# Optimization experiments

Measured on AMD Instinct MI355X. Metric: run time of the kernel, lower is better.

The kernel has to match this reference:

```python
import jax, jax.numpy as jnp
import numpy as np

L = 248      # max_clip_seq_len
WIN = 3      # window_size
H = 8        # attention heads
D = 768      # input/output dim
HID = 256    # rope hidden dim
SIGMA = 2.0
EPS_LN = 1e-5


def _layernorm(x, g, b):
    m = jnp.mean(x, axis=-1, keepdims=True)
    v = jnp.var(x, axis=-1, keepdims=True)
    return (x - m) / jnp.sqrt(v + EPS_LN) * g + b


def _normalize(x):
    n = jnp.linalg.norm(x, axis=-1, keepdims=True)
    return x / jnp.maximum(n, 1e-12)


def _peb_forward(word_feat, text_feat_full, word_pos, ctx_W, ctx_b, in_W, in_b,
                 out_W, out_b, cn_g, cn_b, r1_W, r1_b, ln_g, ln_b, r2_W, r2_b,
                 pos_emb, pos_temp):
    B, N, _ = word_feat.shape
    valid = word_pos != -1                              # [B,N] bool
    vf = valid.astype(word_feat.dtype)[..., None]       # [B,N,1]
    wp = jnp.clip(word_pos, 0, L - 1)                   # [B,N]
    half = WIN // 2
    offs = jnp.arange(-half, half + 1)
    positions = jnp.clip(wp[..., None] + offs[None, None, :], 0, L - 1)
    ctx = text_feat_full[jnp.arange(B)[:, None, None], positions]
    ctx_anchor = (ctx.reshape(B, N, WIN * D) @ ctx_W + ctx_b) * vf       # [B,N,D]
    q = word_feat * vf                                  # word_proj is Identity (768->768)
    # MultiheadAttention (batch_first), query=q, key=value=ctx_anchor
    hd = D // H
    qp = (q @ in_W[:, :D] + in_b[:D]).reshape(B, N, H, hd)
    kp = (ctx_anchor @ in_W[:, D:2 * D] + in_b[D:2 * D]).reshape(B, N, H, hd)
    vp = (ctx_anchor @ in_W[:, 2 * D:] + in_b[2 * D:]).reshape(B, N, H, hd)
    scores = jnp.einsum('bqhd,bkhd->bhqk', qp, kp) / jnp.sqrt(jnp.asarray(hd, q.dtype))
    attn = jax.nn.softmax(scores, axis=-1)
    ao = jnp.einsum('bhqk,bkhd->bqhd', attn, vp).reshape(B, N, D)
    attn_out = ao @ out_W + out_b
    x = _layernorm(q + attn_out, cn_g, cn_b) * vf       # word_feat_with_ctx
    # rope_mapping: Linear -> GELU -> LayerNorm -> Linear
    rope = _layernorm(jax.nn.gelu(x @ r1_W + r1_b, approximate=False), ln_g, ln_b) @ r2_W + r2_b
    rope_n = _normalize(rope)
    clip_ref_n = _normalize(pos_emb)                    # [L,D]
    temp = jnp.maximum(pos_temp, 0.001)
    logits = jnp.einsum('bnd,ld->bnl', rope_n, clip_ref_n) / temp
    log_q = jax.nn.log_softmax(logits, axis=-1)
    # gaussian soft target over L positions
    pos_idx = jnp.arange(L, dtype=jnp.float32)
    d2 = (pos_idx[None, None, :] - wp[..., None].astype(jnp.float32)) ** 2
    targ = jnp.exp(-d2 / (2.0 * SIGMA ** 2))
    targ = targ / (targ.sum(axis=-1, keepdims=True) + 1e-12)
    lqv = log_q * vf
    tv = targ * vf
    n_valid = valid.sum().astype(jnp.float32)
    safe_t = jnp.where(tv > 0, tv, 1.0)
    kl = jnp.sum(jnp.where(tv > 0, tv * (jnp.log(safe_t) - lqv), 0.0)) / (n_valid + 1e-12)
    # relative position loss on cosine similarity
    pos_sim01 = (jnp.einsum('bnd,bmd->bnm', rope_n, rope_n) + 1.0) / 2.0
    wpf = wp.astype(jnp.float32)
    target_sim = 1.0 - jnp.abs(wpf[:, :, None] - wpf[:, None, :]) / float(L)
    vm2 = vf[:, :, 0][:, None, :] * vf[:, :, 0][:, :, None]
    rel = jnp.sum((pos_sim01 * vm2 - target_sim * vm2) ** 2) / (vm2.sum() + 1e-12)
    peb_loss = (1.0 * kl + 0.5 * rel) * 1.0             # kl_weight=1, rel_weight=0.5, peb_weight=1
    # scatter blended positional features to 248-length sequence (vectorized over batch)
    vals = 0.8 * pos_emb[wp] + 0.2 * rope               # [B,N,D]
    pos_s = jnp.where(valid, wp, L)                     # invalid -> OOB index, dropped
    emb = jnp.zeros((B, L, D), word_feat.dtype).at[jnp.arange(B)[:, None], pos_s].set(vals, mode='drop')
    return emb, peb_loss, kl, rel


def setup_inputs() -> dict:
    key = jax.random.key(0)
    ks = jax.random.split(key, 20)
    B, N = 128, 128
    word_feat = jax.random.normal(ks[0], (B, N, D), jnp.float32)
    text_feat_full = jax.random.normal(ks[1], (B, L, D), jnp.float32)
    # unique sorted positions per batch (scatter is then deterministic, matching torch)
    perms = jax.vmap(lambda k: jax.random.permutation(k, L))(jax.random.split(ks[2], B))
    word_pos = jnp.sort(perms[:, :N], axis=-1).astype(jnp.int32)
    s = 0.02
    return {
        'word_feat': word_feat,
        'text_feat_full': text_feat_full,
        'word_pos': word_pos,
        'ctx_W': s * jax.random.normal(ks[3], (WIN * D, D), jnp.float32),
        'ctx_b': s * jax.random.normal(ks[4], (D,), jnp.float32),
        'in_W': s * jax.random.normal(ks[5], (D, 3 * D), jnp.float32),
        'in_b': s * jax.random.normal(ks[6], (3 * D,), jnp.float32),
        'out_W': s * jax.random.normal(ks[7], (D, D), jnp.float32),
        'out_b': s * jax.random.normal(ks[8], (D,), jnp.float32),
        'cn_g': jnp.ones((D,), jnp.float32) + s * jax.random.normal(ks[9], (D,), jnp.float32),
        'cn_b': s * jax.random.normal(ks[10], (D,), jnp.float32),
        'r1_W': s * jax.random.normal(ks[11], (D, HID), jnp.float32),
        'r1_b': s * jax.random.normal(ks[12], (HID,), jnp.float32),
        'ln_g': jnp.ones((HID,), jnp.float32) + s * jax.random.normal(ks[13], (HID,), jnp.float32),
        'ln_b': s * jax.random.normal(ks[14], (HID,), jnp.float32),
        'r2_W': s * jax.random.normal(ks[15], (HID, D), jnp.float32),
        'r2_b': s * jax.random.normal(ks[16], (D,), jnp.float32),
        'pos_emb': jax.random.normal(ks[17], (L, D), jnp.float32),
        'pos_temp': jnp.asarray(1.0, jnp.float32),
    }


def reference(word_feat, text_feat_full, word_pos, ctx_W, ctx_b, in_W, in_b,
              out_W, out_b, cn_g, cn_b, r1_W, r1_b, ln_g, ln_b, r2_W, r2_b,
              pos_emb, pos_temp):
    return _peb_forward(word_feat, text_feat_full, word_pos, ctx_W, ctx_b, in_W, in_b,
                        out_W, out_b, cn_g, cn_b, r1_W, r1_b, ln_g, ln_b, r2_W, r2_b,
                        pos_emb, pos_temp)
```

## Files before the change

kernel.cpp:

```cpp
#include <hip/hip_runtime.h>
#include <math.h>

#define BB   128
#define NN   128
#define LL   248
#define DD   768
#define HH   8
#define HDh  96
#define HIDN 256
#define MROWS (BB*NN)
#define MB_   (1u<<20)
#define KVLD 1536

typedef unsigned short u16;
typedef unsigned int   u32;
typedef __attribute__((ext_vector_type(8))) short s16x8;
typedef __attribute__((ext_vector_type(4))) float f32x4;

__device__ __forceinline__ u16 f2bf(float x) {
    u32 u = __float_as_uint(x);
    u32 r = u + 0x7fffu + ((u >> 16) & 1u);
    return (u16)(r >> 16);
}
__device__ __forceinline__ float bf2f(u16 h) {
    return __uint_as_float(((u32)h) << 16);
}
__device__ __forceinline__ void gload16(const void* g, void* l) {
    __builtin_amdgcn_global_load_lds(
        (const __attribute__((address_space(1))) void*)g,
        (__attribute__((address_space(3))) void*)l, 16, 0, 0);
}

template<int NT>
__device__ __forceinline__ float breduce_sum(float v, float* red) {
    const int tid = threadIdx.x;
    red[tid] = v; __syncthreads();
#pragma unroll
    for (int o = NT / 2; o > 0; o >>= 1) {
        if (tid < o) red[tid] += red[tid + o];
        __syncthreads();
    }
    float r = red[0]; __syncthreads();
    return r;
}
__device__ __forceinline__ double breduce_sum_d256(double v, double* red) {
    const int tid = threadIdx.x;
    red[tid] = v; __syncthreads();
#pragma unroll
    for (int o = 128; o > 0; o >>= 1) {
        if (tid < o) red[tid] += red[tid + o];
        __syncthreads();
    }
    double r = red[0]; __syncthreads();
    return r;
}

#define TEXT_F4 (BB*LL*DD/4)
#define Q_F4    (MROWS*(DD/4))
__global__ __launch_bounds__(256)
void prep_all_kernel(const float* __restrict__ ctx_W, u16* __restrict__ ctx_Wt,
                     const float* __restrict__ in_W,  u16* __restrict__ in_Wt,
                     const float* __restrict__ out_W, u16* __restrict__ out_Wt,
                     const float* __restrict__ r1_W,  u16* __restrict__ r1_Wt,
                     const float* __restrict__ r2_W,  u16* __restrict__ r2_Wt,
                     const float* __restrict__ text,  u16* __restrict__ textb,
                     const float* __restrict__ wf,    u16* __restrict__ qb,
                     const int* __restrict__ wpos,    int* __restrict__ cpos,
                     const float* __restrict__ pe,    u16* __restrict__ clipb,
                     float* __restrict__ zbias) {
    __shared__ float smem[32 * 33];
    int bid = blockIdx.x;
    const int tid = threadIdx.x;

    if (bid < 4416) {
        const float* src; u16* dst; int C;
        if (bid < 1728)      { src = ctx_W; dst = ctx_Wt; C = 768;  }
        else if (bid < 3456) { src = in_W;  dst = in_Wt;  C = 2304; bid -= 1728; }
        else if (bid < 4032) { src = out_W; dst = out_Wt; C = 768;  bid -= 3456; }
        else if (bid < 4224) { src = r1_W;  dst = r1_Wt;  C = 256;  bid -= 4032; }
        else                 { src = r2_W;  dst = r2_Wt;  C = 768;  bid -= 4224; }
        const int R = (C == 768) ? ((dst == ctx_Wt) ? 2304 : ((dst == out_Wt) ? 768 : 256))
                                 : 768;
        const int ct = C >> 5;
        const int r0 = (bid / ct) * 32, c0 = (bid % ct) * 32;
        const int tx = tid & 31, ty = tid >> 5;
#pragma unroll
        for (int i = 0; i < 32; i += 8)
            smem[(ty + i) * 33 + tx] = src[(size_t)(r0 + ty + i) * C + c0 + tx];
        __syncthreads();
#pragma unroll
        for (int i = 0; i < 32; i += 8)
            dst[(size_t)(c0 + ty + i) * R + r0 + tx] = f2bf(smem[tx * 33 + ty + i]);
    } else if (bid < 4672) {
        const int l = bid - 4416;
        if (l >= LL) {
            for (int j = 0; j < 3; ++j) clipb[(size_t)l * DD + tid + j * 256] = 0;
            return;
        }
        float t[3]; float q = 0.f;
#pragma unroll
        for (int j = 0; j < 3; ++j) {
            t[j] = pe[(size_t)l * DD + tid + j * 256];
            q = fmaf(t[j], t[j], q);
        }
        q = breduce_sum<256>(q, smem);
        float inv = 1.f / fmaxf(sqrtf(q), 1e-12f);
#pragma unroll
        for (int j = 0; j < 3; ++j)
            clipb[(size_t)l * DD + tid + j * 256] = f2bf(t[j] * inv);
    } else {
        const int ebid = bid - 4672;
        if (ebid == 0) {
            for (int r = tid; r < MROWS; r += 256) {
                int w = wpos[r];
                cpos[r] = w < 0 ? 0 : (w > LL - 1 ? LL - 1 : w);
            }
            if (tid < 256) zbias[tid] = 0.f;
        }
        const int lane = tid & 63;
        const int wid = ebid * 4 + (tid >> 6);
        const int NCHUNK = (TEXT_F4 + Q_F4) / 512;
        for (int c = wid; c < NCHUNK; c += 8192) {
            const int base = c * 512;
            if (base < TEXT_F4) {
                const float4* sp = (const float4*)text;
                uint2* op = (uint2*)textb;
                float4 v[8];
#pragma unroll
                for (int j = 0; j < 8; ++j)
                    v[j] = sp[(size_t)base + j * 64 + lane];
#pragma unroll
                for (int j = 0; j < 8; ++j) {
                    uint2 o;
                    o.x = (u32)f2bf(v[j].x) | ((u32)f2bf(v[j].y) << 16);
                    o.y = (u32)f2bf(v[j].z) | ((u32)f2bf(v[j].w) << 16);
                    op[(size_t)base + j * 64 + lane] = o;
                }
            } else {
                const int qb4 = base - TEXT_F4;
                const float4* sp = (const float4*)wf;
                uint2* op = (uint2*)qb;
                float4 v[8]; float vfm[8];
#pragma unroll
                for (int j = 0; j < 8; ++j)
                    v[j] = sp[(size_t)qb4 + j * 64 + lane];
#pragma unroll
                for (int j = 0; j < 8; ++j)
                    vfm[j] = (wpos[(qb4 + j * 64 + lane) / 192] != -1) ? 1.f : 0.f;
#pragma unroll
                for (int j = 0; j < 8; ++j) {
                    uint2 o;
                    o.x = (u32)f2bf(v[j].x * vfm[j]) | ((u32)f2bf(v[j].y * vfm[j]) << 16);
                    o.y = (u32)f2bf(v[j].z * vfm[j]) | ((u32)f2bf(v[j].w * vfm[j]) << 16);
                    op[(size_t)qb4 + j * 64 + lane] = o;
                }
            }
        }
    }
}

template<int GATHER, int CBF16, int MASK>
__global__ __launch_bounds__(256)
void gemm_bt(const u16* __restrict__ A,
             const u16* __restrict__ TXT,
             const int* __restrict__ cpos,
             const u16* __restrict__ Bt,
             const float* __restrict__ bias,
             void* __restrict__ Cout, int ldc, int K,
             const int* __restrict__ wpos) {
    __shared__ __align__(16) u16 Alds[128 * 64];
    __shared__ __align__(16) u16 Blds[128 * 64];
    const int tid = threadIdx.x;
    const int l = tid & 63, wv = tid >> 6;

    const int gx  = gridDim.x;
    const int hw  = blockIdx.y * gx + blockIdx.x;
    const int nwg = gx * gridDim.y;
    const int cpx = nwg >> 3;
    const int lin = (hw & 7) * cpx + (hw >> 3);
    const int m0 = (lin / gx) * 128, n0 = (lin % gx) * 128;

    const int rw = wv * 8 + (l >> 3);
    const int ce = ((l & 7) ^ (l >> 3)) << 3;
    u16* Ad0 = Alds + wv * 512;
    u16* Bd0 = Blds + wv * 512;

    const int wm = (wv >> 1) * 64, wn = (wv & 1) * 64;
    const int la = l & 15, lg = l >> 4;

    int aoff[4], boff[4];
#pragma unroll
    for (int m = 0; m < 4; ++m) {
        int ra = wm + m * 16 + la;
        aoff[m] = ra * 64 + (((lg ^ (la & 7)) << 3));
        int rb = wn + m * 16 + la;
        boff[m] = rb * 64 + (((lg ^ (la & 7)) << 3));
    }

    const u16* pb[4];
#pragma unroll
    for (int i = 0; i < 4; ++i)
        pb[i] = Bt + (size_t)(n0 + rw + i * 32) * K + ce;

    f32x4 acc[4][4] = {};

    auto do_step = [&](const u16* a0, const u16* a1, const u16* a2, const u16* a3,
                       const u16* b0, const u16* b1, const u16* b2, const u16* b3) {
        gload16(a0, Ad0);
        gload16(a1, Ad0 + 2048);
        gload16(a2, Ad0 + 4096);
        gload16(a3, Ad0 + 6144);
        gload16(b0, Bd0);
        gload16(b1, Bd0 + 2048);
        gload16(b2, Bd0 + 4096);
        gload16(b3, Bd0 + 6144);
        __syncthreads();
#pragma unroll
        for (int kk = 0; kk < 2; ++kk) {
            const int kx = kk << 5;
            s16x8 af[4], bf[4];
#pragma unroll
            for (int m = 0; m < 4; ++m) af[m] = *(const s16x8*)(Alds + (aoff[m] ^ kx));
#pragma unroll
            for (int n = 0; n < 4; ++n) bf[n] = *(const s16x8*)(Blds + (boff[n] ^ kx));
#pragma unroll
            for (int m = 0; m < 4; ++m)
#pragma unroll
                for (int n = 0; n < 4; ++n)
                    acc[m][n] = __builtin_amdgcn_mfma_f32_16x16x32_bf16(
                        af[m], bf[n], acc[m][n], 0, 0, 0);
        }
        __syncthreads();
    };

    if constexpr (GATHER) {
        int gb[4], gc[4];
#pragma unroll
        for (int i = 0; i < 4; ++i) {
            int g = m0 + rw + i * 32;
            gb[i] = g >> 7;
            gc[i] = cpos[g];
        }
#pragma unroll 1
        for (int w = 0; w < 3; ++w) {
            const u16* pa[4];
#pragma unroll
            for (int i = 0; i < 4; ++i) {
                int p = gc[i] + w - 1;
                p = p < 0 ? 0 : (p > LL - 1 ? LL - 1 : p);
                pa[i] = TXT + ((size_t)(gb[i] * LL + p)) * DD + ce;
            }
            const u16* b0 = pb[0] + w * DD; const u16* b1 = pb[1] + w * DD;
            const u16* b2 = pb[2] + w * DD; const u16* b3 = pb[3] + w * DD;
#pragma unroll 1
            for (int kt = 0; kt < 12; ++kt)
                do_step(pa[0] + kt * 64, pa[1] + kt * 64, pa[2] + kt * 64, pa[3] + kt * 64,
                        b0 + kt * 64, b1 + kt * 64, b2 + kt * 64, b3 + kt * 64);
        }
    } else {
        const u16* pa[4];
#pragma unroll
        for (int i = 0; i < 4; ++i)
            pa[i] = A + (size_t)(m0 + rw + i * 32) * K + ce;
        const int nk = K >> 6;
#pragma unroll 1
        for (int kt = 0; kt < nk; ++kt)
            do_step(pa[0] + (kt << 6), pa[1] + (kt << 6), pa[2] + (kt << 6), pa[3] + (kt << 6),
                    pb[0] + (kt << 6), pb[1] + (kt << 6), pb[2] + (kt << 6), pb[3] + (kt << 6));
    }

#pragma unroll
    for (int m = 0; m < 4; ++m) {
        const int rb = m0 + wm + m * 16 + lg * 4;
        float vf[4];
        if constexpr (MASK) {
#pragma unroll
            for (int r = 0; r < 4; ++r) vf[r] = (wpos[rb + r] != -1) ? 1.f : 0.f;
        }
#pragma unroll
        for (int n = 0; n < 4; ++n) {
            const int col = n0 + wn + n * 16 + la;
            const float bv = bias[col];
#pragma unroll
            for (int r = 0; r < 4; ++r) {
                float o = acc[m][n][r] + bv;
                if constexpr (MASK) o *= vf[r];
                if constexpr (CBF16)
                    ((u16*)Cout)[(size_t)(rb + r) * ldc + col] = f2bf(o);
                else
                    ((float*)Cout)[(size_t)(rb + r) * ldc + col] = o;
            }
        }
    }
}

__global__ __launch_bounds__(512)
void attn_mfma_kernel(const u16* __restrict__ qp, const u16* __restrict__ kvb,
                      u16* __restrict__ ao) {
    __shared__ __align__(16) u16 K_lds[128 * 96];
    __shared__ __align__(16) u16 Vt_lds[96 * 128];
    __shared__ __align__(16) u16 P_lds[128 * 128];
    const int bh = blockIdx.x;
    const int b = bh >> 3, h = bh & 7;
    const int tid = threadIdx.x;
    const int l = tid & 63, wv = tid >> 6;
    const int la = l & 15, lg = l >> 4;
    const float scale = 0.10206207261596575f;

    const size_t qbase  = ((size_t)b * NN) * DD + h * HDh;
    const size_t kvbase = ((size_t)b * NN) * KVLD + h * HDh;

#pragma unroll
    for (int i = 0; i < 3; ++i) {
        int f = i * 8192 + wv * 1024 + l * 16;
        int row = f / 192;
        int inner = f - row * 192;
        gload16((const char*)(kvb + kvbase + (size_t)row * KVLD) + inner,
                (char*)K_lds + f);
    }

    uint4 vchunk[3]; int vkey[3], vd0[3];
#pragma unroll
    for (int i = 0; i < 3; ++i) {
        int c = tid + i * 512;
        int key = c / 12, dc = c - key * 12;
        vkey[i] = key; vd0[i] = dc * 8;
        vchunk[i] = *(const uint4*)(kvb + kvbase + (size_t)key * KVLD + DD + dc * 8);
    }

    const int q0 = wv * 16;
    s16x8 qf[3];
#pragma unroll
    for (int kt = 0; kt < 3; ++kt)
        qf[kt] = *(const s16x8*)(qp + qbase + (size_t)(q0 + la) * DD + kt * 32 + lg * 8);

#pragma unroll
    for (int i = 0; i < 3; ++i) {
        const u16* e = (const u16*)&vchunk[i];
#pragma unroll
        for (int j = 0; j < 8; ++j) {
            int d = vd0[i] + j;
            int byte = ((d * 128 + vkey[i]) * 2) ^ ((d & 7) << 4);
            *(u16*)((char*)Vt_lds + byte) = e[j];
        }
    }
    __syncthreads();

    f32x4 sacc[8] = {};
#pragma unroll
    for (int kt = 0; kt < 3; ++kt) {
#pragma unroll
        for (int nf = 0; nf < 8; ++nf) {
            s16x8 bfr = *(const s16x8*)(K_lds + (nf * 16 + la) * 96 + kt * 32 + lg * 8);
            sacc[nf] = __builtin_amdgcn_mfma_f32_16x16x32_bf16(qf[kt], bfr, sacc[nf], 0, 0, 0);
        }
    }

#pragma unroll
    for (int r = 0; r < 4; ++r) {
        float m = -1e30f;
#pragma unroll
        for (int nf = 0; nf < 8; ++nf) m = fmaxf(m, sacc[nf][r]);
#pragma unroll
        for (int o = 8; o > 0; o >>= 1) m = fmaxf(m, __shfl_xor(m, o, 64));
        m *= scale;
        float p[8]; float s = 0.f;
#pragma unroll
        for (int nf = 0; nf < 8; ++nf) { p[nf] = expf(sacc[nf][r] * scale - m); s += p[nf]; }
#pragma unroll
        for (int o = 8; o > 0; o >>= 1) s += __shfl_xor(s, o, 64);
        const float inv = 1.f / s;
        const int q = q0 + lg * 4 + r;
#pragma unroll
        for (int nf = 0; nf < 8; ++nf) {
            int byte = ((q * 128 + nf * 16 + la) * 2) ^ ((q & 7) << 4);
            *(u16*)((char*)P_lds + byte) = f2bf(p[nf] * inv);
        }
    }
    __syncthreads();

    f32x4 oacc[6] = {};
#pragma unroll
    for (int kk = 0; kk < 4; ++kk) {
        const int qrow = q0 + la;
        int abyte = ((qrow * 128 + kk * 32 + lg * 8) * 2) ^ ((qrow & 7) << 4);
        s16x8 af = *(const s16x8*)((char*)P_lds + abyte);
#pragma unroll
        for (int nf = 0; nf < 6; ++nf) {
            const int d = nf * 16 + la;
            int bbyte = ((d * 128 + kk * 32 + lg * 8) * 2) ^ ((d & 7) << 4);
            s16x8 bfr = *(const s16x8*)((char*)Vt_lds + bbyte);
            oacc[nf] = __builtin_amdgcn_mfma_f32_16x16x32_bf16(af, bfr, oacc[nf], 0, 0, 0);
        }
    }

#pragma unroll
    for (int nf = 0; nf < 6; ++nf) {
#pragma unroll
        for (int r = 0; r < 4; ++r) {
            const int q = q0 + lg * 4 + r;
            ao[qbase + (size_t)q * DD + nf * 16 + la] = f2bf(oacc[nf][r]);
        }
    }
}

__global__ __launch_bounds__(256)
void ln768_kernel(const u16* __restrict__ qb, const u16* __restrict__ at,
                  const int* __restrict__ wpos, const float* __restrict__ g,
                  const float* __restrict__ bta, u16* __restrict__ xout) {
    __shared__ float red[256];
    const int r = blockIdx.x, tid = threadIdx.x;
    const float vf = (wpos[r] != -1) ? 1.f : 0.f;
    float t[3]; float s = 0.f, q = 0.f;
#pragma unroll
    for (int j = 0; j < 3; ++j) {
        int d = tid + j * 256;
        t[j] = bf2f(qb[(size_t)r * DD + d]) + bf2f(at[(size_t)r * DD + d]);
        s += t[j];
        q = fmaf(t[j], t[j], q);
    }
    s = breduce_sum<256>(s, red);
    q = breduce_sum<256>(q, red);
    float mean = s * (1.f / DD);
    float var  = q * (1.f / DD) - mean * mean;
    float inv  = 1.f / sqrtf(var + 1e-5f);
#pragma unroll
    for (int j = 0; j < 3; ++j) {
        int d = tid + j * 256;
        xout[(size_t)r * DD + d] = f2bf(((t[j] - mean) * inv * g[d] + bta[d]) * vf);
    }
}

__global__ __launch_bounds__(256)
void ln256_gelu_kernel(const u16* __restrict__ g1, const float* __restrict__ lg,
                       const float* __restrict__ lb, u16* __restrict__ hout) {
    __shared__ float red[256];
    const int r = blockIdx.x, tid = threadIdx.x;
    float v  = bf2f(g1[(size_t)r * HIDN + tid]);
    float ge = 0.5f * v * (1.f + erff(v * 0.7071067811865475f));
    float s = breduce_sum<256>(ge, red);
    float q = breduce_sum<256>(ge * ge, red);
    float mean = s * (1.f / HIDN);
    float var  = q * (1.f / HIDN) - mean * mean;
    float inv  = 1.f / sqrtf(var + 1e-5f);
    hout[(size_t)r * HIDN + tid] = f2bf((ge - mean) * inv * lg[tid] + lb[tid]);
}

__global__ __launch_bounds__(256)
void norm_rnb_kernel(const u16* __restrict__ ropeb, u16* __restrict__ rnb) {
    __shared__ float red[256];
    const int r = blockIdx.x, tid = threadIdx.x;
    float t[3]; float q = 0.f;
#pragma unroll
    for (int j = 0; j < 3; ++j) {
        t[j] = bf2f(ropeb[(size_t)r * DD + tid + j * 256]);
        q = fmaf(t[j], t[j], q);
    }
    q = breduce_sum<256>(q, red);
    float inv = 1.f / fmaxf(sqrtf(q), 1e-12f);
#pragma unroll
    for (int j = 0; j < 3; ++j)
        rnb[(size_t)r * DD + tid + j * 256] = f2bf(t[j] * inv);
}

__global__ __launch_bounds__(256)
void emb_full_kernel(const u16* __restrict__ ropeb, const float* __restrict__ pe,
                     const int* __restrict__ wpos, float* __restrict__ emb) {
    const int bl = blockIdx.x;
    const int b = bl / LL, l = bl - b * LL;
    const int tid = threadIdx.x;
    const int* wp = wpos + b * NN;
    int lo = 0, hi = NN - 1, found = -1;
    while (lo <= hi) {
        int mid = (lo + hi) >> 1;
        int v = wp[mid];
        if (v == l) { found = mid; break; }
        if (v < l) lo = mid + 1; else hi = mid - 1;
    }
    float* dst = emb + (size_t)bl * DD;
    if (found >= 0) {
        const u16* rr = ropeb + (size_t)(b * NN + found) * DD;
#pragma unroll
        for (int j = 0; j < 3; ++j) {
            int d = tid + j * 256;
            dst[d] = 0.8f * pe[(size_t)l * DD + d] + 0.2f * bf2f(rr[d]);
        }
    } else {
#pragma unroll
        for (int j = 0; j < 3; ++j)
            dst[tid + j * 256] = 0.f;
    }
}

__global__ __launch_bounds__(256)
void kl_lite_kernel(const float* __restrict__ logits, const int* __restrict__ wpos,
                    const float* __restrict__ pos_temp, float* __restrict__ klp) {
    const int row = blockIdx.x * 4 + (threadIdx.x >> 6);
    const int l = threadIdx.x & 63;
    const float invt = 1.f / fmaxf(pos_temp[0], 0.001f);
    const float* lrow = logits + (size_t)row * 256;

    float lg[4];
#pragma unroll
    for (int q = 0; q < 4; ++q) {
        int c = l + q * 64;
        lg[q] = (c < LL) ? lrow[c] * invt : -1e30f;
    }
    float m = fmaxf(fmaxf(lg[0], lg[1]), fmaxf(lg[2], lg[3]));
#pragma unroll
    for (int o = 32; o > 0; o >>= 1) m = fmaxf(m, __shfl_xor(m, o, 64));

    float S = 0.f;
#pragma unroll
    for (int q = 0; q < 4; ++q) S += expf(lg[q] - m);
#pragma unroll
    for (int o = 32; o > 0; o >>= 1) S += __shfl_xor(S, o, 64);
    const float logZ = m + logf(S);

    const int wr = wpos[row];
    const bool valid = (wr != -1);
    const int wp = wr < 0 ? 0 : (wr > LL - 1 ? LL - 1 : wr);

    float targ[4]; float tsum = 0.f;
#pragma unroll
    for (int q = 0; q < 4; ++q) {
        int c = l + q * 64;
        float dl = (float)c - (float)wp;
        targ[q] = (c < LL) ? expf(-dl * dl * 0.125f) : 0.f;
        tsum += targ[q];
    }
#pragma unroll
    for (int o = 32; o > 0; o >>= 1) tsum += __shfl_xor(tsum, o, 64);
    const float tden = 1.f / (tsum + 1e-12f);

    float c_ = 0.f;
#pragma unroll
    for (int q = 0; q < 4; ++q) {
        float tn = targ[q] * tden;
        if (valid && tn > 0.f) c_ += tn * (logf(tn) - (lg[q] - logZ));
    }
#pragma unroll
    for (int o = 32; o > 0; o >>= 1) c_ += __shfl_xor(c_, o, 64);
    if (l == 0) klp[row] = c_;
}

__global__ __launch_bounds__(512)
void rel_mfma_kernel(const u16* __restrict__ rnb, const int* __restrict__ wpos,
                     float* __restrict__ rel_part, float* __restrict__ vm2_part) {
    __shared__ __align__(16) u16 T[128 * 32];
    __shared__ float red[512];
    const int blk = blockIdx.x;
    const int b = blk >> 1, jh = blk & 1;
    const int tid = threadIdx.x;
    const int l = tid & 63, wv = tid >> 6;
    const int la = l & 15, lg = l >> 4;

    const int f = wv * 1024 + l * 16;
    const int rA = f >> 6;
    const int cb = (f & 63) ^ (((rA >> 1) & 3) << 4);
    const int ce = cb >> 1;
    const u16* src = rnb + ((size_t)(b * NN + rA)) * DD + ce;
    u16* dst = T + wv * 512;

    const int ra = wv * 16 + la;
    const int aoff = ra * 32 + ((lg * 8) ^ (((ra >> 1) & 3) << 3));
    int boff[4];
#pragma unroll
    for (int nf = 0; nf < 4; ++nf) {
        int rb = jh * 64 + nf * 16 + la;
        boff[nf] = rb * 32 + ((lg * 8) ^ (((rb >> 1) & 3) << 3));
    }

    f32x4 acc[4] = {};
    for (int kt = 0; kt < 24; ++kt) {
        gload16(src + kt * 32, dst);
        __syncthreads();
        s16x8 a = *(const s16x8*)(T + aoff);
        s16x8 bf_[4];
#pragma unroll
        for (int nf = 0; nf < 4; ++nf) bf_[nf] = *(const s16x8*)(T + boff[nf]);
#pragma unroll
        for (int nf = 0; nf < 4; ++nf)
            acc[nf] = __builtin_amdgcn_mfma_f32_16x16x32_bf16(a, bf_[nf], acc[nf], 0, 0, 0);
        __syncthreads();
    }

    float wif[4], vi[4];
#pragma unroll
    for (int r = 0; r < 4; ++r) {
        int wi = wpos[b * NN + wv * 16 + lg * 4 + r];
        vi[r] = (wi != -1) ? 1.f : 0.f;
        wif[r] = (float)(wi < 0 ? 0 : (wi > LL - 1 ? LL - 1 : wi));
    }
    float csum = 0.f, msum = 0.f;
#pragma unroll
    for (int nf = 0; nf < 4; ++nf) {
        int wj = wpos[b * NN + jh * 64 + nf * 16 + la];
        float vj = (wj != -1) ? 1.f : 0.f;
        float wjf = (float)(wj < 0 ? 0 : (wj > LL - 1 ? LL - 1 : wj));
#pragma unroll
        for (int r = 0; r < 4; ++r) {
            float sim = (acc[nf][r] + 1.f) * 0.5f;
            float ts  = 1.f - fabsf(wif[r] - wjf) * (1.f / (float)LL);
            float m2  = vi[r] * vj;
            float df  = m2 * (sim - ts);
            csum += df * df;
            msum += m2;
        }
    }
    csum = breduce_sum<512>(csum, red);
    msum = breduce_sum<512>(msum, red);
    if (tid == 0) { rel_part[blk] = csum; vm2_part[blk] = msum; }
}

__global__ __launch_bounds__(256)
void final_kernel(const float* __restrict__ klp, const float* __restrict__ relp,
                  const float* __restrict__ vmp, const int* __restrict__ wpos,
                  float* __restrict__ outs) {
    __shared__ double rd[256];
    const int tid = threadIdx.x;
    double kl = 0.0, rel = 0.0, vm = 0.0, nv = 0.0;
    for (int r = tid; r < MROWS; r += 256) {
        kl += (double)klp[r];
        nv += (wpos[r] != -1) ? 1.0 : 0.0;
    }
    if (tid < 256) {
        rel += (double)relp[tid];
        vm  += (double)vmp[tid];
    }
    kl  = breduce_sum_d256(kl, rd);
    rel = breduce_sum_d256(rel, rd);
    vm  = breduce_sum_d256(vm, rd);
    nv  = breduce_sum_d256(nv, rd);
    if (tid == 0) {
        float klf  = (float)(kl / (nv + 1e-12));
        float relf = (float)(rel / (vm + 1e-12));
        outs[0] = klf + 0.5f * relf;
        outs[1] = klf;
        outs[2] = relf;
    }
}

extern "C" void kernel_launch(void* const* d_in, const int* in_sizes, int n_in,
                              void* d_out, int out_size, void* d_ws, size_t ws_size,
                              hipStream_t stream) {
    (void)in_sizes; (void)n_in; (void)ws_size; (void)out_size;

    const float* word_feat = (const float*)d_in[0];
    const float* text      = (const float*)d_in[1];
    const int*   wpos      = (const int*)d_in[2];
    const float* ctx_W     = (const float*)d_in[3];
    const float* ctx_b     = (const float*)d_in[4];
    const float* in_W      = (const float*)d_in[5];
    const float* in_b      = (const float*)d_in[6];
    const float* out_W     = (const float*)d_in[7];
    const float* out_b     = (const float*)d_in[8];
    const float* cn_g      = (const float*)d_in[9];
    const float* cn_b      = (const float*)d_in[10];
    const float* r1_W      = (const float*)d_in[11];
    const float* r1_b      = (const float*)d_in[12];
    const float* ln_g      = (const float*)d_in[13];
    const float* ln_b      = (const float*)d_in[14];
    const float* r2_W      = (const float*)d_in[15];
    const float* r2_b      = (const float*)d_in[16];
    const float* pos_emb   = (const float*)d_in[17];
    const float* pos_temp  = (const float*)d_in[18];

    char* W = (char*)d_ws;
    u16*   ctx_Wt = (u16*)(W);
    u16*   in_Wt  = ctx_Wt + (size_t)768 * 2304;
    u16*   out_Wt = in_Wt  + (size_t)2304 * 768;
    u16*   r1_Wt  = out_Wt + (size_t)768 * 768;
    u16*   r2_Wt  = r1_Wt  + (size_t)256 * 768;
    u16*   clipb  = r2_Wt + (size_t)768 * 256;
    int*   cposb  = (int*)(clipb + (size_t)256 * DD);
    float* klp    = (float*)(cposb + MROWS);
    float* relp   = klp + MROWS;
    float* vmp    = relp + 256;
    float* zbias  = vmp + 256;
    u16*   textb  = (u16*)(W + (size_t)12 * MB_);
    u16*   atoutb = textb;
    float* logits = (float*)(W + (size_t)12 * MB_);
    u16*   xb     = (u16*)(W + (size_t)36 * MB_);
    u16*   qb     = (u16*)(W + (size_t)60 * MB_);
    u16*   ctxa   = (u16*)(W + (size_t)86 * MB_);
    u16*   aob    = ctxa;
    u16*   rnb    = ctxa;
    u16*   qpb    = (u16*)(W + (size_t)112 * MB_);
    u16*   g1b    = (u16*)(W + (size_t)112 * MB_);
    u16*   hb     = (u16*)(W + (size_t)128 * MB_);
    u16*   kvb    = (u16*)(W + (size_t)138 * MB_);
    u16*   ropeb  = kvb;

    dim3 blk(256);

    prep_all_kernel<<<dim3(4416 + 256 + 2048), blk, 0, stream>>>(
        ctx_W, ctx_Wt, in_W, in_Wt, out_W, out_Wt, r1_W, r1_Wt, r2_W, r2_Wt,
        text, textb, word_feat, qb, wpos, cposb, pos_emb, clipb, zbias);

    dim3 g768(6, 128);
    dim3 g1536(12, 128);
    dim3 g256(2, 128);

    gemm_bt<1, 1, 1><<<g768, blk, 0, stream>>>(
        nullptr, textb, cposb, ctx_Wt, ctx_b, ctxa, DD, 3 * DD, wpos);
    gemm_bt<0, 1, 0><<<g768, blk, 0, stream>>>(
        qb, nullptr, nullptr, in_Wt, in_b, qpb, DD, DD, nullptr);
    gemm_bt<0, 1, 0><<<g1536, blk, 0, stream>>>(
        ctxa, nullptr, nullptr, in_Wt + (size_t)768 * 768, in_b + DD, kvb, KVLD, DD, nullptr);
    attn_mfma_kernel<<<dim3(BB * HH), dim3(512), 0, stream>>>(qpb, kvb, aob);
    gemm_bt<0, 1, 0><<<g768, blk, 0, stream>>>(
        aob, nullptr, nullptr, out_Wt, out_b, atoutb, DD, DD, nullptr);
    ln768_kernel<<<dim3(MROWS), blk, 0, stream>>>(qb, atoutb, wpos, cn_g, cn_b, xb);
    gemm_bt<0, 1, 0><<<g256, blk, 0, stream>>>(
        xb, nullptr, nullptr, r1_Wt, r1_b, g1b, HIDN, DD, nullptr);
    ln256_gelu_kernel<<<dim3(MROWS), blk, 0, stream>>>(g1b, ln_g, ln_b, hb);
    gemm_bt<0, 1, 0><<<g768, blk, 0, stream>>>(
        hb, nullptr, nullptr, r2_Wt, r2_b, ropeb, DD, HIDN, nullptr);
    norm_rnb_kernel<<<dim3(MROWS), blk, 0, stream>>>(ropeb, rnb);
    gemm_bt<0, 0, 0><<<g256, blk, 0, stream>>>(
        rnb, nullptr, nullptr, clipb, zbias, logits, 256, DD, nullptr);
    kl_lite_kernel<<<dim3(MROWS / 4), blk, 0, stream>>>(logits, wpos, pos_temp, klp);
    rel_mfma_kernel<<<dim3(BB * 2), dim3(512), 0, stream>>>(rnb, wpos, relp, vmp);
    emb_full_kernel<<<dim3(BB * LL), blk, 0, stream>>>(
        ropeb, pos_emb, wpos, (float*)d_out);
    final_kernel<<<dim3(1), blk, 0, stream>>>(
        klp, relp, vmp, wpos, (float*)d_out + (size_t)BB * LL * DD);
}
```

Before: 447.9 us.

## Merge independent kernels into shared launches to fill the GPU

Three pairs of independent kernels now share a launch, with the block index choosing the work: the ctx and q-projection GEMMs, row normalization with the embedding output, and the logits GEMM with the relation-similarity reduction. The relation kernel moves from 512 to 256 threads and each wave handles two 16-row groups. The aim is to cut launch count and fill idle CUs when single small GEMMs leave the machine underused. The cost is the heterogeneous blocks imbalancing each other, and the emb write now runs before the logits rather than overlapping later work.

```diff
diff --git a/kernel.cpp b/kernel.cpp
--- a/kernel.cpp
+++ b/kernel.cpp
@@ -160,25 +160,18 @@
 }
 
 template<int GATHER, int CBF16, int MASK>
-__global__ __launch_bounds__(256)
-void gemm_bt(const u16* __restrict__ A,
-             const u16* __restrict__ TXT,
-             const int* __restrict__ cpos,
-             const u16* __restrict__ Bt,
-             const float* __restrict__ bias,
-             void* __restrict__ Cout, int ldc, int K,
-             const int* __restrict__ wpos) {
-    __shared__ __align__(16) u16 Alds[128 * 64];
-    __shared__ __align__(16) u16 Blds[128 * 64];
+__device__ __forceinline__ void gemm_tile(
+    const int m0, const int n0,
+    const u16* __restrict__ A,
+    const u16* __restrict__ TXT,
+    const int* __restrict__ cpos,
+    const u16* __restrict__ Bt,
+    const float* __restrict__ bias,
+    void* __restrict__ Cout, int ldc, int K,
+    const int* __restrict__ wpos,
+    u16* Alds, u16* Blds) {
     const int tid = threadIdx.x;
     const int l = tid & 63, wv = tid >> 6;
-
-    const int gx  = gridDim.x;
-    const int hw  = blockIdx.y * gx + blockIdx.x;
-    const int nwg = gx * gridDim.y;
-    const int cpx = nwg >> 3;
-    const int lin = (hw & 7) * cpx + (hw >> 3);
-    const int m0 = (lin / gx) * 128, n0 = (lin % gx) * 128;
 
     const int rw = wv * 8 + (l >> 3);
     const int ce = ((l & 7) ^ (l >> 3)) << 3;
@@ -291,6 +284,152 @@
                     ((float*)Cout)[(size_t)(rb + r) * ldc + col] = o;
             }
         }
+    }
+}
+
+template<int GATHER, int CBF16, int MASK>
+__global__ __launch_bounds__(256)
+void gemm_bt(const u16* __restrict__ A,
+             const u16* __restrict__ TXT,
+             const int* __restrict__ cpos,
+             const u16* __restrict__ Bt,
+             const float* __restrict__ bias,
+             void* __restrict__ Cout, int ldc, int K,
+             const int* __restrict__ wpos) {
+    __shared__ __align__(16) u16 Alds[128 * 64];
+    __shared__ __align__(16) u16 Blds[128 * 64];
+    const int gx  = gridDim.x;
+    const int hw  = blockIdx.y * gx + blockIdx.x;
+    const int nwg = gx * gridDim.y;
+    const int cpx = nwg >> 3;
+    const int lin = (hw & 7) * cpx + (hw >> 3);
+    const int m0 = (lin / gx) * 128, n0 = (lin % gx) * 128;
+    gemm_tile<GATHER, CBF16, MASK>(m0, n0, A, TXT, cpos, Bt, bias,
+                                   Cout, ldc, K, wpos, Alds, Blds);
+}
+
+__global__ __launch_bounds__(256)
+void gemm_ctx_qp_kernel(const u16* __restrict__ textb, const int* __restrict__ cpos,
+                        const u16* __restrict__ ctx_Wt, const float* __restrict__ ctx_b,
+                        u16* __restrict__ ctxa,
+                        const u16* __restrict__ qb, const u16* __restrict__ in_Wt,
+                        const float* __restrict__ in_b, u16* __restrict__ qpb,
+                        const int* __restrict__ wpos) {
+    __shared__ __align__(16) u16 Alds[128 * 64];
+    __shared__ __align__(16) u16 Blds[128 * 64];
+    const int bid = blockIdx.x;
+    if (bid < 768) {
+        const int lin = (bid & 7) * 96 + (bid >> 3);
+        const int m0 = (lin / 6) * 128, n0 = (lin % 6) * 128;
+        gemm_tile<1, 1, 1>(m0, n0, nullptr, textb, cpos, ctx_Wt, ctx_b,
+                           ctxa, DD, 3 * DD, wpos, Alds, Blds);
+    } else {
+        const int b2 = bid - 768;
+        const int lin = (b2 & 7) * 96 + (b2 >> 3);
+        const int m0 = (lin / 6) * 128, n0 = (lin % 6) * 128;
+        gemm_tile<0, 1, 0>(m0, n0, qb, nullptr, nullptr, in_Wt, in_b,
+                           qpb, DD, DD, nullptr, Alds, Blds);
+    }
+}
+
+__device__ __forceinline__ void rel_tile(int blk, const u16* __restrict__ rnb,
+                                         const int* __restrict__ wpos,
+                                         float* __restrict__ rel_part,
+                                         float* __restrict__ vm2_part,
+                                         u16* T ) {
+    float* red = (float*)(T + 4096);
+    const int b = blk >> 1, jh = blk & 1;
+    const int tid = threadIdx.x;
+    const int l = tid & 63, wv = tid >> 6;
+    const int la = l & 15, lg = l >> 4;
+
+    const int f0 = wv * 1024 + l * 16;
+    const int f1 = f0 + 4096;
+    const int rA0 = f0 >> 6, rA1 = f1 >> 6;
+    const int ce0 = ((f0 & 63) ^ (((rA0 >> 1) & 3) << 4)) >> 1;
+    const int ce1 = ((f1 & 63) ^ (((rA1 >> 1) & 3) << 4)) >> 1;
+    const u16* src0 = rnb + ((size_t)(b * NN + rA0)) * DD + ce0;
+    const u16* src1 = rnb + ((size_t)(b * NN + rA1)) * DD + ce1;
+    u16* dst0 = T + wv * 512;
+    u16* dst1 = T + 2048 + wv * 512;
+
+    int aoff[2];
+#pragma unroll
+    for (int g = 0; g < 2; ++g) {
+        int ra = wv * 32 + g * 16 + la;
+        aoff[g] = ra * 32 + ((lg * 8) ^ (((ra >> 1) & 3) << 3));
+    }
+    int boff[4];
+#pragma unroll
+    for (int nf = 0; nf < 4; ++nf) {
+        int rb = jh * 64 + nf * 16 + la;
+        boff[nf] = rb * 32 + ((lg * 8) ^ (((rb >> 1) & 3) << 3));
+    }
+
+    f32x4 acc[2][4] = {};
+    for (int kt = 0; kt < 24; ++kt) {
+        gload16(src0 + kt * 32, dst0);
+        gload16(src1 + kt * 32, dst1);
+        __syncthreads();
+        s16x8 a[2], bf_[4];
+#pragma unroll
+        for (int g = 0; g < 2; ++g) a[g] = *(const s16x8*)(T + aoff[g]);
+#pragma unroll
+        for (int nf = 0; nf < 4; ++nf) bf_[nf] = *(const s16x8*)(T + boff[nf]);
+#pragma unroll
+        for (int g = 0; g < 2; ++g)
+#pragma unroll
+            for (int nf = 0; nf < 4; ++nf)
+                acc[g][nf] = __builtin_amdgcn_mfma_f32_16x16x32_bf16(
+                    a[g], bf_[nf], acc[g][nf], 0, 0, 0);
+        __syncthreads();
+    }
+
+    float csum = 0.f, msum = 0.f;
+#pragma unroll
+    for (int g = 0; g < 2; ++g) {
+        float wif[4], vi[4];
+#pragma unroll
+        for (int r = 0; r < 4; ++r) {
+            int wi = wpos[b * NN + wv * 32 + g * 16 + lg * 4 + r];
+            vi[r] = (wi != -1) ? 1.f : 0.f;
+            wif[r] = (float)(wi < 0 ? 0 : (wi > LL - 1 ? LL - 1 : wi));
+        }
+#pragma unroll
+        for (int nf = 0; nf < 4; ++nf) {
+            int wj = wpos[b * NN + jh * 64 + nf * 16 + la];
+            float vj = (wj != -1) ? 1.f : 0.f;
+            float wjf = (float)(wj < 0 ? 0 : (wj > LL - 1 ? LL - 1 : wj));
+#pragma unroll
+            for (int r = 0; r < 4; ++r) {
+                float sim = (acc[g][nf][r] + 1.f) * 0.5f;
+                float ts  = 1.f - fabsf(wif[r] - wjf) * (1.f / (float)LL);
+                float m2  = vi[r] * vj;
+                float df  = m2 * (sim - ts);
+                csum += df * df;
+                msum += m2;
+            }
+        }
+    }
+    csum = breduce_sum<256>(csum, red);
+    msum = breduce_sum<256>(msum, red);
+    if (tid == 0) { rel_part[blk] = csum; vm2_part[blk] = msum; }
+}
+
+__global__ __launch_bounds__(256)
+void logits_rel_kernel(const u16* __restrict__ rnb, const u16* __restrict__ clipb,
+                       const float* __restrict__ zbias, float* __restrict__ logits,
+                       const int* __restrict__ wpos,
+                       float* __restrict__ relp, float* __restrict__ vmp) {
+    __shared__ __align__(16) u16 pool[2 * 128 * 64];
+    const int bid = blockIdx.x;
+    if (bid < 256) {
+        const int lin = (bid & 7) * 32 + (bid >> 3);
+        const int m0 = (lin >> 1) * 128, n0 = (lin & 1) * 128;
+        gemm_tile<0, 0, 0>(m0, n0, rnb, nullptr, nullptr, clipb, zbias,
+                           logits, 256, DD, nullptr, pool, pool + 128 * 64);
+    } else {
+        rel_tile(bid - 256, rnb, wpos, relp, vmp, pool);
     }
 }
 
@@ -447,48 +586,49 @@
 }
 
 __global__ __launch_bounds__(256)
-void norm_rnb_kernel(const u16* __restrict__ ropeb, u16* __restrict__ rnb) {
+void norm_emb_kernel(const u16* __restrict__ ropeb, const float* __restrict__ pe,
+                     const int* __restrict__ wpos, u16* __restrict__ rnb,
+                     float* __restrict__ emb) {
     __shared__ float red[256];
-    const int r = blockIdx.x, tid = threadIdx.x;
-    float t[3]; float q = 0.f;
-#pragma unroll
-    for (int j = 0; j < 3; ++j) {
-        t[j] = bf2f(ropeb[(size_t)r * DD + tid + j * 256]);
-        q = fmaf(t[j], t[j], q);
-    }
-    q = breduce_sum<256>(q, red);
-    float inv = 1.f / fmaxf(sqrtf(q), 1e-12f);
-#pragma unroll
-    for (int j = 0; j < 3; ++j)
-        rnb[(size_t)r * DD + tid + j * 256] = f2bf(t[j] * inv);
-}
-
-__global__ __launch_bounds__(256)
-void emb_full_kernel(const u16* __restrict__ ropeb, const float* __restrict__ pe,
-                     const int* __restrict__ wpos, float* __restrict__ emb) {
-    const int bl = blockIdx.x;
-    const int b = bl / LL, l = bl - b * LL;
+    const int bid = blockIdx.x;
     const int tid = threadIdx.x;
-    const int* wp = wpos + b * NN;
-    int lo = 0, hi = NN - 1, found = -1;
-    while (lo <= hi) {
-        int mid = (lo + hi) >> 1;
-        int v = wp[mid];
-        if (v == l) { found = mid; break; }
-        if (v < l) lo = mid + 1; else hi = mid - 1;
-    }
-    float* dst = emb + (size_t)bl * DD;
-    if (found >= 0) {
-        const u16* rr = ropeb + (size_t)(b * NN + found) * DD;
+    if (bid < MROWS) {
+        const int r = bid;
+        float t[3]; float q = 0.f;
 #pragma unroll
         for (int j = 0; j < 3; ++j) {
-            int d = tid + j * 256;
-            dst[d] = 0.8f * pe[(size_t)l * DD + d] + 0.2f * bf2f(rr[d]);
-        }
+            t[j] = bf2f(ropeb[(size_t)r * DD + tid + j * 256]);
+            q = fmaf(t[j], t[j], q);
+        }
+        q = breduce_sum<256>(q, red);
+        float inv = 1.f / fmaxf(sqrtf(q), 1e-12f);
+#pragma unroll
+        for (int j = 0; j < 3; ++j)
+            rnb[(size_t)r * DD + tid + j * 256] = f2bf(t[j] * inv);
     } else {
-#pragma unroll
-        for (int j = 0; j < 3; ++j)
-            dst[tid + j * 256] = 0.f;
+        const int bl = bid - MROWS;
+        const int b = bl / LL, l = bl - b * LL;
+        const int* wp = wpos + b * NN;
+        int lo = 0, hi = NN - 1, found = -1;
+        while (lo <= hi) {
+            int mid = (lo + hi) >> 1;
+            int v = wp[mid];
+            if (v == l) { found = mid; break; }
+            if (v < l) lo = mid + 1; else hi = mid - 1;
+        }
+        float* dst = emb + (size_t)bl * DD;
+        if (found >= 0) {
+            const u16* rr = ropeb + (size_t)(b * NN + found) * DD;
+#pragma unroll
+            for (int j = 0; j < 3; ++j) {
+                int d = tid + j * 256;
+                dst[d] = 0.8f * pe[(size_t)l * DD + d] + 0.2f * bf2f(rr[d]);
+            }
+        } else {
+#pragma unroll
+            for (int j = 0; j < 3; ++j)
+                dst[tid + j * 256] = 0.f;
+        }
     }
 }
 
@@ -542,75 +682,6 @@
 #pragma unroll
     for (int o = 32; o > 0; o >>= 1) c_ += __shfl_xor(c_, o, 64);
     if (l == 0) klp[row] = c_;
-}
-
-__global__ __launch_bounds__(512)
-void rel_mfma_kernel(const u16* __restrict__ rnb, const int* __restrict__ wpos,
-                     float* __restrict__ rel_part, float* __restrict__ vm2_part) {
-    __shared__ __align__(16) u16 T[128 * 32];
-    __shared__ float red[512];
-    const int blk = blockIdx.x;
-    const int b = blk >> 1, jh = blk & 1;
-    const int tid = threadIdx.x;
-    const int l = tid & 63, wv = tid >> 6;
-    const int la = l & 15, lg = l >> 4;
-
-    const int f = wv * 1024 + l * 16;
-    const int rA = f >> 6;
-    const int cb = (f & 63) ^ (((rA >> 1) & 3) << 4);
-    const int ce = cb >> 1;
-    const u16* src = rnb + ((size_t)(b * NN + rA)) * DD + ce;
-    u16* dst = T + wv * 512;
-
-    const int ra = wv * 16 + la;
-    const int aoff = ra * 32 + ((lg * 8) ^ (((ra >> 1) & 3) << 3));
-    int boff[4];
-#pragma unroll
-    for (int nf = 0; nf < 4; ++nf) {
-        int rb = jh * 64 + nf * 16 + la;
-        boff[nf] = rb * 32 + ((lg * 8) ^ (((rb >> 1) & 3) << 3));
-    }
-
-    f32x4 acc[4] = {};
-    for (int kt = 0; kt < 24; ++kt) {
-        gload16(src + kt * 32, dst);
-        __syncthreads();
-        s16x8 a = *(const s16x8*)(T + aoff);
-        s16x8 bf_[4];
-#pragma unroll
-        for (int nf = 0; nf < 4; ++nf) bf_[nf] = *(const s16x8*)(T + boff[nf]);
-#pragma unroll
-        for (int nf = 0; nf < 4; ++nf)
-            acc[nf] = __builtin_amdgcn_mfma_f32_16x16x32_bf16(a, bf_[nf], acc[nf], 0, 0, 0);
-        __syncthreads();
-    }
-
-    float wif[4], vi[4];
-#pragma unroll
-    for (int r = 0; r < 4; ++r) {
-        int wi = wpos[b * NN + wv * 16 + lg * 4 + r];
-        vi[r] = (wi != -1) ? 1.f : 0.f;
-        wif[r] = (float)(wi < 0 ? 0 : (wi > LL - 1 ? LL - 1 : wi));
-    }
-    float csum = 0.f, msum = 0.f;
-#pragma unroll
-    for (int nf = 0; nf < 4; ++nf) {
-        int wj = wpos[b * NN + jh * 64 + nf * 16 + la];
-        float vj = (wj != -1) ? 1.f : 0.f;
-        float wjf = (float)(wj < 0 ? 0 : (wj > LL - 1 ? LL - 1 : wj));
-#pragma unroll
-        for (int r = 0; r < 4; ++r) {
-            float sim = (acc[nf][r] + 1.f) * 0.5f;
-            float ts  = 1.f - fabsf(wif[r] - wjf) * (1.f / (float)LL);
-            float m2  = vi[r] * vj;
-            float df  = m2 * (sim - ts);
-            csum += df * df;
-            msum += m2;
-        }
-    }
-    csum = breduce_sum<512>(csum, red);
-    msum = breduce_sum<512>(msum, red);
-    if (tid == 0) { rel_part[blk] = csum; vm2_part[blk] = msum; }
 }
 
 __global__ __launch_bounds__(256)
@@ -700,30 +771,25 @@
 
     dim3 g768(6, 128);
     dim3 g1536(12, 128);
-    dim3 g256(2, 128);
-
-    gemm_bt<1, 1, 1><<<g768, blk, 0, stream>>>(
-        nullptr, textb, cposb, ctx_Wt, ctx_b, ctxa, DD, 3 * DD, wpos);
-    gemm_bt<0, 1, 0><<<g768, blk, 0, stream>>>(
-        qb, nullptr, nullptr, in_Wt, in_b, qpb, DD, DD, nullptr);
+
+    gemm_ctx_qp_kernel<<<dim3(1536), blk, 0, stream>>>(
+        textb, cposb, ctx_Wt, ctx_b, ctxa, qb, in_Wt, in_b, qpb, wpos);
     gemm_bt<0, 1, 0><<<g1536, blk, 0, stream>>>(
         ctxa, nullptr, nullptr, in_Wt + (size_t)768 * 768, in_b + DD, kvb, KVLD, DD, nullptr);
     attn_mfma_kernel<<<dim3(BB * HH), dim3(512), 0, stream>>>(qpb, kvb, aob);
     gemm_bt<0, 1, 0><<<g768, blk, 0, stream>>>(
         aob, nullptr, nullptr, out_Wt, out_b, atoutb, DD, DD, nullptr);
     ln768_kernel<<<dim3(MROWS), blk, 0, stream>>>(qb, atoutb, wpos, cn_g, cn_b, xb);
-    gemm_bt<0, 1, 0><<<g256, blk, 0, stream>>>(
+    gemm_bt<0, 1, 0><<<dim3(2, 128), blk, 0, stream>>>(
         xb, nullptr, nullptr, r1_Wt, r1_b, g1b, HIDN, DD, nullptr);
     ln256_gelu_kernel<<<dim3(MROWS), blk, 0, stream>>>(g1b, ln_g, ln_b, hb);
     gemm_bt<0, 1, 0><<<g768, blk, 0, stream>>>(
         hb, nullptr, nullptr, r2_Wt, r2_b, ropeb, DD, HIDN, nullptr);
-    norm_rnb_kernel<<<dim3(MROWS), blk, 0, stream>>>(ropeb, rnb);
-    gemm_bt<0, 0, 0><<<g256, blk, 0, stream>>>(
-        rnb, nullptr, nullptr, clipb, zbias, logits, 256, DD, nullptr);
+    norm_emb_kernel<<<dim3(MROWS + BB * LL), blk, 0, stream>>>(
+        ropeb, pos_emb, wpos, rnb, (float*)d_out);
+    logits_rel_kernel<<<dim3(512), blk, 0, stream>>>(
+        rnb, clipb, zbias, logits, wpos, relp, vmp);
     kl_lite_kernel<<<dim3(MROWS / 4), blk, 0, stream>>>(logits, wpos, pos_temp, klp);
-    rel_mfma_kernel<<<dim3(BB * 2), dim3(512), 0, stream>>>(rnb, wpos, relp, vmp);
-    emb_full_kernel<<<dim3(BB * LL), blk, 0, stream>>>(
-        ropeb, pos_emb, wpos, (float*)d_out);
     final_kernel<<<dim3(1), blk, 0, stream>>>(
         klp, relp, vmp, wpos, (float*)d_out + (size_t)BB * LL * DD);
 }
```

Measured after the change: 433.1 us. -3.3%, faster.
